# Kernel tuning notes

Hardware: AMD Instinct MI355X
Metric: run time of the kernel (lower is better)

## Reference

```python
import jax, jax.numpy as jnp
import numpy as np

D_MODEL = 1024
N_LAYERS = 2
D_INNER = 2048   # expand_factor * d_model
D_STATE = 16
DT_RANK = 64     # ceil(d_model/16)
D_CONV = 4
BATCH = 2
SEQ = 1024
EPS = 1e-5


def setup_inputs() -> dict:
    key = jax.random.key(0)
    ks = jax.random.split(key, 8)
    s = 0.02
    x = jax.random.normal(ks[0], (BATCH, SEQ, D_MODEL), jnp.float32)
    norm_w = jnp.ones((N_LAYERS, D_MODEL), jnp.float32)
    in_proj_w = jax.random.normal(ks[1], (N_LAYERS, 2 * D_INNER, D_MODEL), jnp.float32) * s
    conv_w = jax.random.normal(ks[2], (N_LAYERS, D_INNER, D_CONV), jnp.float32) * s  # depthwise kernel
    conv_b = jnp.zeros((N_LAYERS, D_INNER), jnp.float32)
    x_proj_w = jax.random.normal(ks[3], (N_LAYERS, DT_RANK + 2 * D_STATE, D_INNER), jnp.float32) * s
    dt_std = DT_RANK ** -0.5
    dt_proj_w = jax.random.uniform(ks[4], (N_LAYERS, D_INNER, DT_RANK), jnp.float32, -dt_std, dt_std)
    dt = jnp.exp(jax.random.uniform(ks[5], (N_LAYERS, D_INNER), jnp.float32)
                 * (np.log(0.1) - np.log(0.001)) + np.log(0.001))
    dt = jnp.clip(dt, 1e-4)
    dt_proj_b = dt + jnp.log(-jnp.expm1(-dt))  # inverse softplus init
    A_log = jnp.broadcast_to(jnp.log(jnp.arange(1, D_STATE + 1, dtype=jnp.float32)),
                             (N_LAYERS, D_INNER, D_STATE)).copy()
    D_param = jnp.ones((N_LAYERS, D_INNER), jnp.float32)
    out_proj_w = jax.random.normal(ks[6], (N_LAYERS, D_MODEL, D_INNER), jnp.float32) * s
    return dict(x=x, norm_w=norm_w, in_proj_w=in_proj_w, conv_w=conv_w, conv_b=conv_b,
                x_proj_w=x_proj_w, dt_proj_w=dt_proj_w, dt_proj_b=dt_proj_b,
                A_log=A_log, D_param=D_param, out_proj_w=out_proj_w)


def _rms_norm(x, w):
    return x * jax.lax.rsqrt(jnp.mean(x * x, axis=-1, keepdims=True) + EPS) * w


def _silu(x):
    return x * jax.nn.sigmoid(x)


def _mamba_block(x, in_w, cw, cb, xp_w, dt_w, dt_b, A_log, Dp, out_w):
    # x: (B, L, D)
    xz = x @ in_w.T                      # (B, L, 2*ED)
    xc, z = jnp.split(xz, 2, axis=-1)    # each (B, L, ED)
    # causal depthwise conv1d (torch pads d_conv-1 both sides then slices [:L])
    xpad = jnp.pad(xc, ((0, 0), (D_CONV - 1, 0), (0, 0)))
    L = xc.shape[1]
    xc = sum(xpad[:, k:k + L, :] * cw[:, k] for k in range(D_CONV)) + cb
    xc = _silu(xc)
    # projections for delta, B, C
    dbc = xc @ xp_w.T                    # (B, L, dt_rank + 2N)
    delta = dbc[..., :DT_RANK]
    Bm = dbc[..., DT_RANK:DT_RANK + D_STATE]
    Cm = dbc[..., DT_RANK + D_STATE:]
    delta = jax.nn.softplus(delta @ dt_w.T + dt_b)      # (B, L, ED)
    A = -jnp.exp(A_log)                                 # (ED, N)
    dA = jnp.exp(delta[..., None] * A)                  # (B, L, ED, N)
    bx = (delta * xc)[..., None] * Bm[:, :, None, :]    # (B, L, ED, N)

    def combine(e1, e2):
        a1, b1 = e1
        a2, b2 = e2
        return a2 * a1, a2 * b1 + b2

    _, hs = jax.lax.associative_scan(combine, (dA, bx), axis=1)  # h_t = dA_t*h_{t-1} + bx_t
    y = jnp.einsum('blen,bln->ble', hs, Cm) + Dp * xc
    return (y * _silu(z)) @ out_w.T


def reference(x, norm_w, in_proj_w, conv_w, conv_b, x_proj_w, dt_proj_w, dt_proj_b,
              A_log, D_param, out_proj_w):
    for i in range(N_LAYERS):
        h = _rms_norm(x, norm_w[i])
        x = x + _mamba_block(h, in_proj_w[i], conv_w[i], conv_b[i], x_proj_w[i],
                             dt_proj_w[i], dt_proj_b[i], A_log[i], D_param[i], out_proj_w[i])
    return x
```

## Files before the change

kernel.cpp:

```cpp
#include <hip/hip_runtime.h>
#include <hip/hip_bf16.h>

#define BATCH   2
#define SEQ     1024
#define DMODEL  1024
#define DINNER  2048
#define DSTATE  16
#define DTRANK  64
#define DCONV   4
#define NLAYERS 2
#define ROWS    (BATCH*SEQ)
#define NCHUNK  32
#define CHUNK   32
#define KSPLIT  8
#define KSLICE  (DINNER / KSPLIT)
#define KSO     4
#define KSLICE_O (DINNER / KSO)

typedef unsigned short ushort_t;
typedef __attribute__((ext_vector_type(8))) short short8;
typedef __attribute__((ext_vector_type(4))) float f32x4;

__device__ __forceinline__ ushort_t f2bf(float f) {
  union { float f; unsigned u; } v; v.f = f;
  unsigned r = v.u + 0x7fffu + ((v.u >> 16) & 1u);
  return (ushort_t)(r >> 16);
}
__device__ __forceinline__ float bf2f(ushort_t h) {
  union { unsigned u; float f; } v; v.u = ((unsigned)h) << 16;
  return v.f;
}

__device__ __forceinline__ void g2lds16(const ushort_t* g, ushort_t* l) {
  __builtin_amdgcn_global_load_lds(
      (const __attribute__((address_space(1))) void*)g,
      (__attribute__((address_space(3))) void*)l, 16, 0, 0);
}

__device__ __forceinline__ void xcd_swz(int& bx, int& by) {
  const int nx = gridDim.x, nwg = nx * gridDim.y;
  int id = by * nx + bx;
  const int q = nwg >> 3;
  id = (id & 7) * q + (id >> 3);
  bx = id % nx; by = id / nx;
}

#define STG_Q(tid) (((tid) & 3) ^ (((tid) >> 3) & 3))
#define LDQ(lane)  ((((lane) >> 4) ^ (((lane) >> 1) & 3)) * 8)

__global__ __launch_bounds__(256) void cast_bf16_kernel(
    const float* __restrict__ in, ushort_t* __restrict__ out)
{
  const int i = blockIdx.x * 256 + threadIdx.x;
  const float4 v = reinterpret_cast<const float4*>(in)[i];
  ushort4 o;
  o.x = f2bf(v.x); o.y = f2bf(v.y); o.z = f2bf(v.z); o.w = f2bf(v.w);
  reinterpret_cast<ushort4*>(out)[i] = o;
}

__global__ __launch_bounds__(256) void rmsnorm_kernel(
    const float* __restrict__ x, const float* __restrict__ w,
    ushort_t* __restrict__ out)
{
  const int row = blockIdx.x;
  const float* xr = x + (size_t)row * DMODEL;
  float ss = 0.f;
  #pragma unroll
  for (int i = threadIdx.x; i < DMODEL; i += 256) { float v = xr[i]; ss += v * v; }
  #pragma unroll
  for (int m = 1; m < 64; m <<= 1) ss += __shfl_xor(ss, m);
  __shared__ float red[4];
  if ((threadIdx.x & 63) == 0) red[threadIdx.x >> 6] = ss;
  __syncthreads();
  float tot = red[0] + red[1] + red[2] + red[3];
  float scale = rsqrtf(tot * (1.f / DMODEL) + 1e-5f);
  #pragma unroll
  for (int i = threadIdx.x; i < DMODEL; i += 256)
    out[(size_t)row * DMODEL + i] = f2bf(xr[i] * scale * w[i]);
}

template<int MODE>
__global__ __launch_bounds__(256) void gemm_bf16_kernel(
    const ushort_t* __restrict__ A, const ushort_t* __restrict__ B,
    ushort_t* __restrict__ C2, const float* __restrict__ bias,
    int K, int lda, int ldb, int ldc)
{
  __shared__ __align__(16) ushort_t As[128 * 32];
  __shared__ __align__(16) ushort_t Bs[128 * 32];
  const int tid = threadIdx.x;
  const int lane = tid & 63, wid = tid >> 6;
  const int wr = wid >> 1, wc = wid & 1;
  int bx = blockIdx.x, by = blockIdx.y;
  xcd_swz(bx, by);
  const int row0 = by * 128, col0 = bx * 128;

  const int sq = STG_Q(tid) * 8;
  const ushort_t* ga0 = A + (size_t)(row0 + (tid >> 2)) * lda + sq;
  const ushort_t* ga1 = A + (size_t)(row0 + 64 + (tid >> 2)) * lda + sq;
  const ushort_t* gb0 = B + (size_t)(col0 + (tid >> 2)) * ldb + sq;
  const ushort_t* gb1 = B + (size_t)(col0 + 64 + (tid >> 2)) * ldb + sq;
  ushort_t* la0 = &As[tid * 8];
  ushort_t* la1 = &As[(256 + tid) * 8];
  ushort_t* lb0 = &Bs[tid * 8];
  ushort_t* lb1 = &Bs[(256 + tid) * 8];

  const int lk = LDQ(lane);
  const int lr16 = lane & 15;

  f32x4 acc[4][4] = {};

  for (int kb = 0; kb < K; kb += 32) {
    g2lds16(ga0 + kb, la0);
    g2lds16(ga1 + kb, la1);
    g2lds16(gb0 + kb, lb0);
    g2lds16(gb1 + kb, lb1);
    __syncthreads();

    short8 af[4], bfr[4];
    #pragma unroll
    for (int i = 0; i < 4; ++i)
      af[i] = *reinterpret_cast<const short8*>(
          &As[(wr * 64 + i * 16 + lr16) * 32 + lk]);
    #pragma unroll
    for (int j = 0; j < 4; ++j)
      bfr[j] = *reinterpret_cast<const short8*>(
          &Bs[(wc * 64 + j * 16 + lr16) * 32 + lk]);
    #pragma unroll
    for (int i = 0; i < 4; ++i)
      #pragma unroll
      for (int j = 0; j < 4; ++j)
        acc[i][j] = __builtin_amdgcn_mfma_f32_16x16x32_bf16(
            af[i], bfr[j], acc[i][j], 0, 0, 0);
    __syncthreads();
  }

  const int cr = (lane >> 4) * 4;
  #pragma unroll
  for (int i = 0; i < 4; ++i) {
    #pragma unroll
    for (int j = 0; j < 4; ++j) {
      const int col = col0 + wc * 64 + j * 16 + lr16;
      #pragma unroll
      for (int r = 0; r < 4; ++r) {
        const int row = row0 + wr * 64 + i * 16 + cr + r;
        float v = acc[i][j][r];
        if (MODE == 3) {
          v += bias[col];
          v = (v > 20.f) ? v : log1pf(__expf(v));
        }
        C2[(size_t)row * ldc + col] = f2bf(v);
      }
    }
  }
}

__global__ __launch_bounds__(256) void outproj_splitk_kernel(
    const ushort_t* __restrict__ A,
    const ushort_t* __restrict__ B,
    ushort_t* __restrict__ partial)
{
  __shared__ __align__(16) ushort_t As[128 * 32];
  __shared__ __align__(16) ushort_t Bs[128 * 32];
  const int tid = threadIdx.x;
  const int lane = tid & 63, wid = tid >> 6;
  const int wr = wid >> 1, wc = wid & 1;
  int bx = blockIdx.x, by = blockIdx.y;
  xcd_swz(bx, by);
  const int row0 = by * 128, col0 = bx * 128;
  const int k0 = blockIdx.z * KSLICE_O;

  const int sq = STG_Q(tid) * 8;
  const ushort_t* ga0 = A + (size_t)(row0 + (tid >> 2)) * DINNER + k0 + sq;
  const ushort_t* ga1 = A + (size_t)(row0 + 64 + (tid >> 2)) * DINNER + k0 + sq;
  const ushort_t* gb0 = B + (size_t)(col0 + (tid >> 2)) * DINNER + k0 + sq;
  const ushort_t* gb1 = B + (size_t)(col0 + 64 + (tid >> 2)) * DINNER + k0 + sq;
  ushort_t* la0 = &As[tid * 8];
  ushort_t* la1 = &As[(256 + tid) * 8];
  ushort_t* lb0 = &Bs[tid * 8];
  ushort_t* lb1 = &Bs[(256 + tid) * 8];

  const int lk = LDQ(lane);
  const int lr16 = lane & 15;

  f32x4 acc[4][4] = {};

  for (int kb = 0; kb < KSLICE_O; kb += 32) {
    g2lds16(ga0 + kb, la0);
    g2lds16(ga1 + kb, la1);
    g2lds16(gb0 + kb, lb0);
    g2lds16(gb1 + kb, lb1);
    __syncthreads();

    short8 af[4], bfr[4];
    #pragma unroll
    for (int i = 0; i < 4; ++i)
      af[i] = *reinterpret_cast<const short8*>(
          &As[(wr * 64 + i * 16 + lr16) * 32 + lk]);
    #pragma unroll
    for (int j = 0; j < 4; ++j)
      bfr[j] = *reinterpret_cast<const short8*>(
          &Bs[(wc * 64 + j * 16 + lr16) * 32 + lk]);
    #pragma unroll
    for (int i = 0; i < 4; ++i)
      #pragma unroll
      for (int j = 0; j < 4; ++j)
        acc[i][j] = __builtin_amdgcn_mfma_f32_16x16x32_bf16(
            af[i], bfr[j], acc[i][j], 0, 0, 0);
    __syncthreads();
  }

  ushort_t* Cz = partial + (size_t)blockIdx.z * ROWS * DMODEL;
  const int cr = (lane >> 4) * 4;
  #pragma unroll
  for (int i = 0; i < 4; ++i) {
    #pragma unroll
    for (int j = 0; j < 4; ++j) {
      const int col = col0 + wc * 64 + j * 16 + lr16;
      #pragma unroll
      for (int r = 0; r < 4; ++r) {
        const int row = row0 + wr * 64 + i * 16 + cr + r;
        Cz[(size_t)row * DMODEL + col] = f2bf(acc[i][j][r]);
      }
    }
  }
}

__global__ __launch_bounds__(256) void outproj_reduce_kernel(
    const ushort_t* __restrict__ partial, float* __restrict__ out)
{
  const int i = blockIdx.x * 256 + threadIdx.x;
  float4 s = reinterpret_cast<float4*>(out)[i];
  #pragma unroll
  for (int z = 0; z < KSO; ++z) {
    const ushort4 p = reinterpret_cast<const ushort4*>(
        partial + (size_t)z * ROWS * DMODEL)[i];
    s.x += bf2f(p.x); s.y += bf2f(p.y); s.z += bf2f(p.z); s.w += bf2f(p.w);
  }
  reinterpret_cast<float4*>(out)[i] = s;
}

__global__ __launch_bounds__(256) void xproj_mfma_kernel(
    const ushort_t* __restrict__ A,
    const ushort_t* __restrict__ B,
    ushort_t* __restrict__ partial)
{
  __shared__ __align__(16) ushort_t As[128 * 32];
  __shared__ __align__(16) ushort_t Bs[96 * 32];
  const int tid = threadIdx.x;
  const int lane = tid & 63, wid = tid >> 6;
  int bx = blockIdx.x, by = blockIdx.y;
  xcd_swz(bx, by);
  const int kz = bx, row0 = by * 128;
  const int k0 = kz * KSLICE;

  const int sq = STG_Q(tid) * 8;
  const ushort_t* ga0 = A + (size_t)(row0 + (tid >> 2)) * DINNER + k0 + sq;
  const ushort_t* ga1 = A + (size_t)(row0 + 64 + (tid >> 2)) * DINNER + k0 + sq;
  const ushort_t* gb0 = B + (size_t)(tid >> 2) * DINNER + k0 + sq;
  const ushort_t* gb1 = B + (size_t)(64 + (tid >> 2)) * DINNER + k0 + sq;
  ushort_t* la0 = &As[tid * 8];
  ushort_t* la1 = &As[(256 + tid) * 8];
  ushort_t* lb0 = &Bs[tid * 8];
  ushort_t* lb1 = &Bs[(256 + tid) * 8];

  const int lk = LDQ(lane);
  const int lr16 = lane & 15;

  f32x4 acc[2][6] = {};

  for (int kb = 0; kb < KSLICE; kb += 32) {
    g2lds16(ga0 + kb, la0);
    g2lds16(ga1 + kb, la1);
    g2lds16(gb0 + kb, lb0);
    if (tid < 128) g2lds16(gb1 + kb, lb1);
    __syncthreads();

    short8 af[2], bfr[6];
    #pragma unroll
    for (int i = 0; i < 2; ++i)
      af[i] = *reinterpret_cast<const short8*>(
          &As[(wid * 32 + i * 16 + lr16) * 32 + lk]);
    #pragma unroll
    for (int j = 0; j < 6; ++j)
      bfr[j] = *reinterpret_cast<const short8*>(
          &Bs[(j * 16 + lr16) * 32 + lk]);
    #pragma unroll
    for (int i = 0; i < 2; ++i)
      #pragma unroll
      for (int j = 0; j < 6; ++j)
        acc[i][j] = __builtin_amdgcn_mfma_f32_16x16x32_bf16(
            af[i], bfr[j], acc[i][j], 0, 0, 0);
    __syncthreads();
  }

  const int cr = (lane >> 4) * 4;
  #pragma unroll
  for (int i = 0; i < 2; ++i) {
    #pragma unroll
    for (int j = 0; j < 6; ++j) {
      const int col = j * 16 + lr16;
      #pragma unroll
      for (int r = 0; r < 4; ++r) {
        const int row = row0 + wid * 32 + i * 16 + cr + r;
        partial[((size_t)kz * ROWS + row) * 96 + col] = f2bf(acc[i][j][r]);
      }
    }
  }
}

__global__ __launch_bounds__(256) void xproj_reduce_kernel(
    const ushort_t* __restrict__ partial, float* __restrict__ dbcBC,
    ushort_t* __restrict__ dl16)
{
  const int idx = blockIdx.x * 256 + threadIdx.x;
  const int row = idx / 96, j = idx % 96;
  float s = 0.f;
  #pragma unroll
  for (int z = 0; z < KSPLIT; ++z)
    s += bf2f(partial[(size_t)z * ROWS * 96 + idx]);
  if (j < DTRANK) dl16[row * DTRANK + j] = f2bf(s);
  else            dbcBC[row * 32 + (j - DTRANK)] = s;
}

__global__ __launch_bounds__(256) void conv_silu_kernel(
    const ushort_t* __restrict__ xz16,
    const float* __restrict__ cw, const float* __restrict__ cb,
    ushort_t* __restrict__ xc16)
{
  const int idx = blockIdx.x * 256 + threadIdx.x;
  const int e0 = (idx * 8) % DINNER;
  const int bl = (idx * 8) / DINNER;
  const int l  = bl % SEQ;
  float acc[8];
  #pragma unroll
  for (int j = 0; j < 8; ++j) acc[j] = cb[e0 + j];
  float4 w4[8];
  #pragma unroll
  for (int j = 0; j < 8; ++j)
    w4[j] = *reinterpret_cast<const float4*>(&cw[(e0 + j) * DCONV]);
  #pragma unroll
  for (int k = 0; k < DCONV; ++k) {
    const int lk = l + k - (DCONV - 1);
    if (lk >= 0) {
      const short8 v = *reinterpret_cast<const short8*>(
          &xz16[(size_t)(bl + k - (DCONV - 1)) * (2 * DINNER) + e0]);
      #pragma unroll
      for (int j = 0; j < 8; ++j) {
        const float wv = (k == 0) ? w4[j].x : (k == 1) ? w4[j].y
                        : (k == 2) ? w4[j].z : w4[j].w;
        acc[j] += bf2f((ushort_t)v[j]) * wv;
      }
    }
  }
  short8 o;
  #pragma unroll
  for (int j = 0; j < 8; ++j) {
    const float v = acc[j] / (1.f + __expf(-acc[j]));
    o[j] = (short)f2bf(v);
  }
  *reinterpret_cast<short8*>(&xc16[(size_t)bl * DINNER + e0]) = o;
}

__global__ __launch_bounds__(256) void scan_chunk_kernel(
    const ushort_t* __restrict__ d16,
    const ushort_t* __restrict__ xc16,
    const float* __restrict__ dbcBC,
    const float* __restrict__ A_log,
    float* __restrict__ Pbuf,
    float* __restrict__ Hbuf)
{
  __shared__ float sB[CHUNK][16];
  const int bc = blockIdx.y;
  const int b = bc / NCHUNK, c = bc % NCHUNK;
  const int e = blockIdx.x * 256 + threadIdx.x;
  const size_t row32 = ((size_t)b * SEQ + c * CHUNK) * 32;
  #pragma unroll
  for (int p = 0; p < (CHUNK * 16) / 256; ++p) {
    const int idx = threadIdx.x + p * 256;
    sB[idx >> 4][idx & 15] = dbcBC[row32 + (idx >> 4) * 32 + (idx & 15)];
  }
  float Aen[16];
  #pragma unroll
  for (int q = 0; q < 4; ++q) {
    const float4 a4 = *reinterpret_cast<const float4*>(&A_log[(size_t)e * 16 + q * 4]);
    Aen[q * 4 + 0] = -__expf(a4.x);
    Aen[q * 4 + 1] = -__expf(a4.y);
    Aen[q * 4 + 2] = -__expf(a4.z);
    Aen[q * 4 + 3] = -__expf(a4.w);
  }
  __syncthreads();

  float h[16];
  #pragma unroll
  for (int n = 0; n < 16; ++n) h[n] = 0.f;
  float sd = 0.f;
  const size_t rowE = ((size_t)b * SEQ + c * CHUNK) * DINNER + e;
  float dv = bf2f(d16[rowE]), xv = bf2f(xc16[rowE]);
  for (int t = 0; t < CHUNK; ++t) {
    float dvn = 0.f, xvn = 0.f;
    if (t + 1 < CHUNK) {
      dvn = bf2f(d16[rowE + (size_t)(t + 1) * DINNER]);
      xvn = bf2f(xc16[rowE + (size_t)(t + 1) * DINNER]);
    }
    const float dxv = dv * xv;
    sd += dv;
    #pragma unroll
    for (int n = 0; n < 16; ++n) {
      const float dA = __expf(dv * Aen[n]);
      h[n] = dA * h[n] + dxv * sB[t][n];
    }
    dv = dvn; xv = xvn;
  }
  const size_t o = ((size_t)bc * DINNER + e) * 16;
  #pragma unroll
  for (int q = 0; q < 4; ++q) {
    float4 pv, hv;
    pv.x = __expf(Aen[q * 4 + 0] * sd);
    pv.y = __expf(Aen[q * 4 + 1] * sd);
    pv.z = __expf(Aen[q * 4 + 2] * sd);
    pv.w = __expf(Aen[q * 4 + 3] * sd);
    hv.x = h[q * 4 + 0]; hv.y = h[q * 4 + 1];
    hv.z = h[q * 4 + 2]; hv.w = h[q * 4 + 3];
    *reinterpret_cast<float4*>(&Pbuf[o + q * 4]) = pv;
    *reinterpret_cast<float4*>(&Hbuf[o + q * 4]) = hv;
  }
}

__global__ __launch_bounds__(256) void scan_combine_kernel(
    const float* __restrict__ Pbuf, float* __restrict__ Hbuf)
{
  const int idx = blockIdx.x * 256 + threadIdx.x;
  const int b = idx >> 15;
  const int en = idx & (DINNER * 16 - 1);
  const size_t base = (size_t)b * NCHUNK * DINNER * 16 + en;
  float H = 0.f;
  float P = Pbuf[base], hf = Hbuf[base];
  for (int c = 0; c < NCHUNK; ++c) {
    const size_t o = base + (size_t)c * DINNER * 16;
    float Pn = 0.f, hfn = 0.f;
    if (c + 1 < NCHUNK) {
      const size_t on = o + (size_t)DINNER * 16;
      Pn = Pbuf[on]; hfn = Hbuf[on];
    }
    Hbuf[o] = H;
    H = P * H + hf;
    P = Pn; hf = hfn;
  }
}

__global__ __launch_bounds__(256) void scan_out_kernel(
    const ushort_t* __restrict__ d16,
    const ushort_t* __restrict__ xc16,
    const float* __restrict__ dbcBC,
    const ushort_t* __restrict__ xz16,
    const float* __restrict__ A_log,
    const float* __restrict__ Dp,
    const float* __restrict__ Hbuf,
    ushort_t* __restrict__ yz16)
{
  __shared__ float sB[CHUNK][16];
  __shared__ float sC[CHUNK][16];
  const int bc = blockIdx.y;
  const int b = bc / NCHUNK, c = bc % NCHUNK;
  const int e = blockIdx.x * 256 + threadIdx.x;
  const size_t row32 = ((size_t)b * SEQ + c * CHUNK) * 32;
  #pragma unroll
  for (int p = 0; p < (CHUNK * 32) / 256; ++p) {
    const int idx = threadIdx.x + p * 256;
    const int t = idx >> 5, j = idx & 31;
    const float v = dbcBC[row32 + t * 32 + j];
    if (j < 16) sB[t][j] = v; else sC[t][j - 16] = v;
  }
  float Aen[16];
  #pragma unroll
  for (int q = 0; q < 4; ++q) {
    const float4 a4 = *reinterpret_cast<const float4*>(&A_log[(size_t)e * 16 + q * 4]);
    Aen[q * 4 + 0] = -__expf(a4.x);
    Aen[q * 4 + 1] = -__expf(a4.y);
    Aen[q * 4 + 2] = -__expf(a4.z);
    Aen[q * 4 + 3] = -__expf(a4.w);
  }
  float h[16];
  const size_t oh = ((size_t)bc * DINNER + e) * 16;
  #pragma unroll
  for (int q = 0; q < 4; ++q) {
    const float4 hv = *reinterpret_cast<const float4*>(&Hbuf[oh + q * 4]);
    h[q * 4 + 0] = hv.x; h[q * 4 + 1] = hv.y;
    h[q * 4 + 2] = hv.z; h[q * 4 + 3] = hv.w;
  }
  const float dpe = Dp[e];
  __syncthreads();

  const size_t rowE = ((size_t)b * SEQ + c * CHUNK) * DINNER + e;
  const size_t rowZ = ((size_t)b * SEQ + c * CHUNK) * (2 * DINNER) + DINNER + e;
  float dv = bf2f(d16[rowE]), xv = bf2f(xc16[rowE]);
  float zv = bf2f(xz16[rowZ]);
  for (int t = 0; t < CHUNK; ++t) {
    float dvn = 0.f, xvn = 0.f, zvn = 0.f;
    if (t + 1 < CHUNK) {
      dvn = bf2f(d16[rowE + (size_t)(t + 1) * DINNER]);
      xvn = bf2f(xc16[rowE + (size_t)(t + 1) * DINNER]);
      zvn = bf2f(xz16[rowZ + (size_t)(t + 1) * (2 * DINNER)]);
    }
    const float dxv = dv * xv;
    float y = dpe * xv;
    #pragma unroll
    for (int n = 0; n < 16; ++n) {
      const float dA = __expf(dv * Aen[n]);
      h[n] = dA * h[n] + dxv * sB[t][n];
      y += h[n] * sC[t][n];
    }
    const float sz = zv / (1.f + __expf(-zv));
    yz16[rowE + (size_t)t * DINNER] = f2bf(y * sz);
    dv = dvn; xv = xvn; zv = zvn;
  }
}

extern "C" void kernel_launch(void* const* d_in, const int* in_sizes, int n_in,
                              void* d_out, int out_size, void* d_ws, size_t ws_size,
                              hipStream_t stream)
{
  const float* x         = (const float*)d_in[0];
  const float* norm_w    = (const float*)d_in[1];
  const float* in_proj_w = (const float*)d_in[2];
  const float* conv_w    = (const float*)d_in[3];
  const float* conv_b    = (const float*)d_in[4];
  const float* x_proj_w  = (const float*)d_in[5];
  const float* dt_proj_w = (const float*)d_in[6];
  const float* dt_proj_b = (const float*)d_in[7];
  const float* A_log     = (const float*)d_in[8];
  const float* D_param   = (const float*)d_in[9];
  const float* out_proj_w= (const float*)d_in[10];
  float* out = (float*)d_out;

  const size_t M = 1024 * 1024;
  float* ws = (float*)d_ws;
  ushort_t* h16   = (ushort_t*)ws;
  ushort_t* w16i  = (ushort_t*)(ws + 1 * M);
  ushort_t* partO = (ushort_t*)ws;
  ushort_t* w16o  = (ushort_t*)(ws + 4 * M);
  ushort_t* xz16  = (ushort_t*)(ws + 5 * M);
  ushort_t* xc16  = (ushort_t*)(ws + 9 * M);
  ushort_t* d16   = (ushort_t*)(ws + 11 * M);
  float* P_buf    = ws + 13 * M;
  ushort_t* yz16  = (ushort_t*)P_buf;
  float* H_buf    = ws + 15 * M;
  ushort_t* partX = (ushort_t*)(ws + 17 * M);
  ushort_t* xpw16 = (ushort_t*)(ws + 17 * M + 786432);
  ushort_t* dtw16 = (ushort_t*)(ws + 17 * M + 786432 + 98304);
  float* dbcBC    = ws + 17 * M + 786432 + 98304 + 65536;
  ushort_t* dl16  = (ushort_t*)(dbcBC + 65536);

  hipMemcpyAsync(out, x, (size_t)ROWS * DMODEL * sizeof(float),
                 hipMemcpyDeviceToDevice, stream);

  for (int layer = 0; layer < NLAYERS; ++layer) {
    const float* nw  = norm_w     + (size_t)layer * DMODEL;
    const float* iw  = in_proj_w  + (size_t)layer * 2 * DINNER * DMODEL;
    const float* cw  = conv_w     + (size_t)layer * DINNER * DCONV;
    const float* cb  = conv_b     + (size_t)layer * DINNER;
    const float* xpw = x_proj_w   + (size_t)layer * 96 * DINNER;
    const float* dtw = dt_proj_w  + (size_t)layer * DINNER * DTRANK;
    const float* dtb = dt_proj_b  + (size_t)layer * DINNER;
    const float* Al  = A_log      + (size_t)layer * DINNER * DSTATE;
    const float* Dpp = D_param    + (size_t)layer * DINNER;
    const float* ow  = out_proj_w + (size_t)layer * DMODEL * DINNER;

    rmsnorm_kernel<<<ROWS, 256, 0, stream>>>(out, nw, h16);

    cast_bf16_kernel<<<(2 * DINNER * DMODEL) / 1024, 256, 0, stream>>>(iw, w16i);

    gemm_bf16_kernel<2>
        <<<dim3(2 * DINNER / 128, ROWS / 128), 256, 0, stream>>>(
            h16, w16i, xz16, nullptr, DMODEL, DMODEL, DMODEL, 2 * DINNER);

    conv_silu_kernel<<<(size_t)ROWS * DINNER / 8 / 256, 256, 0, stream>>>(
        xz16, cw, cb, xc16);

    cast_bf16_kernel<<<(96 * DINNER) / 1024, 256, 0, stream>>>(xpw, xpw16);
    cast_bf16_kernel<<<(DINNER * DTRANK) / 1024, 256, 0, stream>>>(dtw, dtw16);

    xproj_mfma_kernel<<<dim3(KSPLIT, ROWS / 128), 256, 0, stream>>>(
        xc16, xpw16, partX);
    xproj_reduce_kernel<<<ROWS * 96 / 256, 256, 0, stream>>>(
        partX, dbcBC, dl16);

    gemm_bf16_kernel<3>
        <<<dim3(DINNER / 128, ROWS / 128), 256, 0, stream>>>(
            dl16, dtw16, d16, dtb, DTRANK, DTRANK, DTRANK, DINNER);

    scan_chunk_kernel<<<dim3(DINNER / 256, BATCH * NCHUNK), 256, 0, stream>>>(
        d16, xc16, dbcBC, Al, P_buf, H_buf);
    scan_combine_kernel<<<BATCH * DINNER * 16 / 256, 256, 0, stream>>>(
        P_buf, H_buf);
    scan_out_kernel<<<dim3(DINNER / 256, BATCH * NCHUNK), 256, 0, stream>>>(
        d16, xc16, dbcBC, xz16, Al, Dpp, H_buf, yz16);

    cast_bf16_kernel<<<(DMODEL * DINNER) / 1024, 256, 0, stream>>>(ow, w16o);

    outproj_splitk_kernel
        <<<dim3(DMODEL / 128, ROWS / 128, KSO), 256, 0, stream>>>(
            yz16, w16o, partO);
    outproj_reduce_kernel<<<ROWS * DMODEL / 1024, 256, 0, stream>>>(
        partO, out);
  }
}
```

Measured before the change: 344.5 us.

## Fuse RMSNorm into residual reduce, batch weight casts, store scan carries in bf16

Merges the initial copy with the first RMSNorm, and folds each later RMSNorm into the out-projection split-K reduce kernel, so the residual is not read again per layer. All weight casts for both layers are issued up front in four launches instead of per-layer casts. The scan chunk prefix products and carry states are stored as bf16 instead of fp32, halving that scratch traffic at some cost in accuracy of the cross-chunk recurrence. The workspace layout is rearranged to fit the new buffers.

```diff
diff --git a/kernel.cpp b/kernel.cpp
--- a/kernel.cpp
+++ b/kernel.cpp
@@ -58,25 +58,27 @@
   reinterpret_cast<ushort4*>(out)[i] = o;
 }
 
-__global__ __launch_bounds__(256) void rmsnorm_kernel(
+__global__ __launch_bounds__(256) void init_rms_kernel(
     const float* __restrict__ x, const float* __restrict__ w,
-    ushort_t* __restrict__ out)
-{
-  const int row = blockIdx.x;
-  const float* xr = x + (size_t)row * DMODEL;
-  float ss = 0.f;
-  #pragma unroll
-  for (int i = threadIdx.x; i < DMODEL; i += 256) { float v = xr[i]; ss += v * v; }
+    float* __restrict__ out, ushort_t* __restrict__ h16)
+{
+  const int row = blockIdx.x, t = threadIdx.x;
+  const size_t base = (size_t)row * DMODEL + 4 * t;
+  const float4 s = *reinterpret_cast<const float4*>(&x[base]);
+  *reinterpret_cast<float4*>(&out[base]) = s;
+  float ss = s.x * s.x + s.y * s.y + s.z * s.z + s.w * s.w;
   #pragma unroll
   for (int m = 1; m < 64; m <<= 1) ss += __shfl_xor(ss, m);
   __shared__ float red[4];
-  if ((threadIdx.x & 63) == 0) red[threadIdx.x >> 6] = ss;
+  if ((t & 63) == 0) red[t >> 6] = ss;
   __syncthreads();
-  float tot = red[0] + red[1] + red[2] + red[3];
-  float scale = rsqrtf(tot * (1.f / DMODEL) + 1e-5f);
-  #pragma unroll
-  for (int i = threadIdx.x; i < DMODEL; i += 256)
-    out[(size_t)row * DMODEL + i] = f2bf(xr[i] * scale * w[i]);
+  const float tot = red[0] + red[1] + red[2] + red[3];
+  const float scale = rsqrtf(tot * (1.f / DMODEL) + 1e-5f);
+  const float4 w4 = *reinterpret_cast<const float4*>(&w[4 * t]);
+  ushort4 o;
+  o.x = f2bf(s.x * scale * w4.x); o.y = f2bf(s.y * scale * w4.y);
+  o.z = f2bf(s.z * scale * w4.z); o.w = f2bf(s.w * scale * w4.w);
+  *reinterpret_cast<ushort4*>(&h16[base]) = o;
 }
 
 template<int MODE>
@@ -225,18 +227,36 @@
   }
 }
 
-__global__ __launch_bounds__(256) void outproj_reduce_kernel(
-    const ushort_t* __restrict__ partial, float* __restrict__ out)
-{
-  const int i = blockIdx.x * 256 + threadIdx.x;
-  float4 s = reinterpret_cast<float4*>(out)[i];
+template<bool RMS>
+__global__ __launch_bounds__(256) void outproj_reduce_rms_kernel(
+    const ushort_t* __restrict__ partial, const float* __restrict__ nw,
+    float* __restrict__ out, ushort_t* __restrict__ h16)
+{
+  const int row = blockIdx.x, t = threadIdx.x;
+  const size_t base = (size_t)row * DMODEL + 4 * t;
+  float4 s = *reinterpret_cast<float4*>(&out[base]);
   #pragma unroll
   for (int z = 0; z < KSO; ++z) {
-    const ushort4 p = reinterpret_cast<const ushort4*>(
-        partial + (size_t)z * ROWS * DMODEL)[i];
+    const ushort4 p = *reinterpret_cast<const ushort4*>(
+        &partial[(size_t)z * ROWS * DMODEL + base]);
     s.x += bf2f(p.x); s.y += bf2f(p.y); s.z += bf2f(p.z); s.w += bf2f(p.w);
   }
-  reinterpret_cast<float4*>(out)[i] = s;
+  *reinterpret_cast<float4*>(&out[base]) = s;
+  if (RMS) {
+    float ss = s.x * s.x + s.y * s.y + s.z * s.z + s.w * s.w;
+    #pragma unroll
+    for (int m = 1; m < 64; m <<= 1) ss += __shfl_xor(ss, m);
+    __shared__ float red[4];
+    if ((t & 63) == 0) red[t >> 6] = ss;
+    __syncthreads();
+    const float tot = red[0] + red[1] + red[2] + red[3];
+    const float scale = rsqrtf(tot * (1.f / DMODEL) + 1e-5f);
+    const float4 w4 = *reinterpret_cast<const float4*>(&nw[4 * t]);
+    ushort4 o;
+    o.x = f2bf(s.x * scale * w4.x); o.y = f2bf(s.y * scale * w4.y);
+    o.z = f2bf(s.z * scale * w4.z); o.w = f2bf(s.w * scale * w4.w);
+    *reinterpret_cast<ushort4*>(&h16[base]) = o;
+  }
 }
 
 __global__ __launch_bounds__(256) void xproj_mfma_kernel(
@@ -366,8 +386,8 @@
     const ushort_t* __restrict__ xc16,
     const float* __restrict__ dbcBC,
     const float* __restrict__ A_log,
-    float* __restrict__ Pbuf,
-    float* __restrict__ Hbuf)
+    ushort_t* __restrict__ P16,
+    ushort_t* __restrict__ H16)
 {
   __shared__ float sB[CHUNK][16];
   const int bc = blockIdx.y;
@@ -414,35 +434,35 @@
   const size_t o = ((size_t)bc * DINNER + e) * 16;
   #pragma unroll
   for (int q = 0; q < 4; ++q) {
-    float4 pv, hv;
-    pv.x = __expf(Aen[q * 4 + 0] * sd);
-    pv.y = __expf(Aen[q * 4 + 1] * sd);
-    pv.z = __expf(Aen[q * 4 + 2] * sd);
-    pv.w = __expf(Aen[q * 4 + 3] * sd);
-    hv.x = h[q * 4 + 0]; hv.y = h[q * 4 + 1];
-    hv.z = h[q * 4 + 2]; hv.w = h[q * 4 + 3];
-    *reinterpret_cast<float4*>(&Pbuf[o + q * 4]) = pv;
-    *reinterpret_cast<float4*>(&Hbuf[o + q * 4]) = hv;
+    ushort4 pv, hv;
+    pv.x = f2bf(__expf(Aen[q * 4 + 0] * sd));
+    pv.y = f2bf(__expf(Aen[q * 4 + 1] * sd));
+    pv.z = f2bf(__expf(Aen[q * 4 + 2] * sd));
+    pv.w = f2bf(__expf(Aen[q * 4 + 3] * sd));
+    hv.x = f2bf(h[q * 4 + 0]); hv.y = f2bf(h[q * 4 + 1]);
+    hv.z = f2bf(h[q * 4 + 2]); hv.w = f2bf(h[q * 4 + 3]);
+    *reinterpret_cast<ushort4*>(&P16[o + q * 4]) = pv;
+    *reinterpret_cast<ushort4*>(&H16[o + q * 4]) = hv;
   }
 }
 
 __global__ __launch_bounds__(256) void scan_combine_kernel(
-    const float* __restrict__ Pbuf, float* __restrict__ Hbuf)
+    const ushort_t* __restrict__ P16, ushort_t* __restrict__ H16)
 {
   const int idx = blockIdx.x * 256 + threadIdx.x;
   const int b = idx >> 15;
   const int en = idx & (DINNER * 16 - 1);
   const size_t base = (size_t)b * NCHUNK * DINNER * 16 + en;
   float H = 0.f;
-  float P = Pbuf[base], hf = Hbuf[base];
+  float P = bf2f(P16[base]), hf = bf2f(H16[base]);
   for (int c = 0; c < NCHUNK; ++c) {
     const size_t o = base + (size_t)c * DINNER * 16;
     float Pn = 0.f, hfn = 0.f;
     if (c + 1 < NCHUNK) {
       const size_t on = o + (size_t)DINNER * 16;
-      Pn = Pbuf[on]; hfn = Hbuf[on];
-    }
-    Hbuf[o] = H;
+      Pn = bf2f(P16[on]); hfn = bf2f(H16[on]);
+    }
+    H16[o] = f2bf(H);
     H = P * H + hf;
     P = Pn; hf = hfn;
   }
@@ -455,7 +475,7 @@
     const ushort_t* __restrict__ xz16,
     const float* __restrict__ A_log,
     const float* __restrict__ Dp,
-    const float* __restrict__ Hbuf,
+    const ushort_t* __restrict__ H16,
     ushort_t* __restrict__ yz16)
 {
   __shared__ float sB[CHUNK][16];
@@ -484,9 +504,9 @@
   const size_t oh = ((size_t)bc * DINNER + e) * 16;
   #pragma unroll
   for (int q = 0; q < 4; ++q) {
-    const float4 hv = *reinterpret_cast<const float4*>(&Hbuf[oh + q * 4]);
-    h[q * 4 + 0] = hv.x; h[q * 4 + 1] = hv.y;
-    h[q * 4 + 2] = hv.z; h[q * 4 + 3] = hv.w;
+    const ushort4 hv = *reinterpret_cast<const ushort4*>(&H16[oh + q * 4]);
+    h[q * 4 + 0] = bf2f(hv.x); h[q * 4 + 1] = bf2f(hv.y);
+    h[q * 4 + 2] = bf2f(hv.z); h[q * 4 + 3] = bf2f(hv.w);
   }
   const float dpe = Dp[e];
   __syncthreads();
@@ -535,40 +555,43 @@
 
   const size_t M = 1024 * 1024;
   float* ws = (float*)d_ws;
-  ushort_t* h16   = (ushort_t*)ws;
-  ushort_t* w16i  = (ushort_t*)(ws + 1 * M);
-  ushort_t* partO = (ushort_t*)ws;
-  ushort_t* w16o  = (ushort_t*)(ws + 4 * M);
-  ushort_t* xz16  = (ushort_t*)(ws + 5 * M);
-  ushort_t* xc16  = (ushort_t*)(ws + 9 * M);
-  ushort_t* d16   = (ushort_t*)(ws + 11 * M);
-  float* P_buf    = ws + 13 * M;
-  ushort_t* yz16  = (ushort_t*)P_buf;
-  float* H_buf    = ws + 15 * M;
-  ushort_t* partX = (ushort_t*)(ws + 17 * M);
-  ushort_t* xpw16 = (ushort_t*)(ws + 17 * M + 786432);
-  ushort_t* dtw16 = (ushort_t*)(ws + 17 * M + 786432 + 98304);
-  float* dbcBC    = ws + 17 * M + 786432 + 98304 + 65536;
-  ushort_t* dl16  = (ushort_t*)(dbcBC + 65536);
-
-  hipMemcpyAsync(out, x, (size_t)ROWS * DMODEL * sizeof(float),
-                 hipMemcpyDeviceToDevice, stream);
+  ushort_t* w16i_all = (ushort_t*)ws;
+  ushort_t* w16o_all = (ushort_t*)(ws + 4 * M);
+  ushort_t* xpw16_all= (ushort_t*)(ws + 6 * M);
+  ushort_t* dtw16_all= (ushort_t*)(ws + 6 * M + 196608);
+  float* dbcBC    = ws + 6 * M + 327680;
+  ushort_t* dl16  = (ushort_t*)(ws + 6 * M + 393216);
+  ushort_t* xz16  = (ushort_t*)(ws + 6 * M + 524288);
+  ushort_t* partO = xz16;
+  ushort_t* xc16  = (ushort_t*)(ws + 10 * M + 524288);
+  ushort_t* d16   = (ushort_t*)(ws + 12 * M + 524288);
+  ushort_t* P16   = (ushort_t*)(ws + 14 * M + 524288);
+  ushort_t* H16   = (ushort_t*)(ws + 15 * M + 524288);
+  ushort_t* yz16  = (ushort_t*)(ws + 16 * M + 524288);
+  ushort_t* h16   = (ushort_t*)(ws + 18 * M + 524288);
+  ushort_t* partX = (ushort_t*)(ws + 19 * M + 524288);
+
+  cast_bf16_kernel<<<NLAYERS * 2 * DINNER * DMODEL / 1024, 256, 0, stream>>>(
+      in_proj_w, w16i_all);
+  cast_bf16_kernel<<<NLAYERS * DMODEL * DINNER / 1024, 256, 0, stream>>>(
+      out_proj_w, w16o_all);
+  cast_bf16_kernel<<<NLAYERS * 96 * DINNER / 1024, 256, 0, stream>>>(
+      x_proj_w, xpw16_all);
+  cast_bf16_kernel<<<NLAYERS * DINNER * DTRANK / 1024, 256, 0, stream>>>(
+      dt_proj_w, dtw16_all);
+
+  init_rms_kernel<<<ROWS, 256, 0, stream>>>(x, norm_w, out, h16);
 
   for (int layer = 0; layer < NLAYERS; ++layer) {
-    const float* nw  = norm_w     + (size_t)layer * DMODEL;
-    const float* iw  = in_proj_w  + (size_t)layer * 2 * DINNER * DMODEL;
     const float* cw  = conv_w     + (size_t)layer * DINNER * DCONV;
     const float* cb  = conv_b     + (size_t)layer * DINNER;
-    const float* xpw = x_proj_w   + (size_t)layer * 96 * DINNER;
-    const float* dtw = dt_proj_w  + (size_t)layer * DINNER * DTRANK;
     const float* dtb = dt_proj_b  + (size_t)layer * DINNER;
     const float* Al  = A_log      + (size_t)layer * DINNER * DSTATE;
     const float* Dpp = D_param    + (size_t)layer * DINNER;
-    const float* ow  = out_proj_w + (size_t)layer * DMODEL * DINNER;
-
-    rmsnorm_kernel<<<ROWS, 256, 0, stream>>>(out, nw, h16);
-
-    cast_bf16_kernel<<<(2 * DINNER * DMODEL) / 1024, 256, 0, stream>>>(iw, w16i);
+    const ushort_t* w16i  = w16i_all  + (size_t)layer * 2 * DINNER * DMODEL;
+    const ushort_t* w16o  = w16o_all  + (size_t)layer * DMODEL * DINNER;
+    const ushort_t* xpw16 = xpw16_all + (size_t)layer * 96 * DINNER;
+    const ushort_t* dtw16 = dtw16_all + (size_t)layer * DINNER * DTRANK;
 
     gemm_bf16_kernel<2>
         <<<dim3(2 * DINNER / 128, ROWS / 128), 256, 0, stream>>>(
@@ -576,9 +599,6 @@
 
     conv_silu_kernel<<<(size_t)ROWS * DINNER / 8 / 256, 256, 0, stream>>>(
         xz16, cw, cb, xc16);
-
-    cast_bf16_kernel<<<(96 * DINNER) / 1024, 256, 0, stream>>>(xpw, xpw16);
-    cast_bf16_kernel<<<(DINNER * DTRANK) / 1024, 256, 0, stream>>>(dtw, dtw16);
 
     xproj_mfma_kernel<<<dim3(KSPLIT, ROWS / 128), 256, 0, stream>>>(
         xc16, xpw16, partX);
@@ -590,18 +610,22 @@
             dl16, dtw16, d16, dtb, DTRANK, DTRANK, DTRANK, DINNER);
 
     scan_chunk_kernel<<<dim3(DINNER / 256, BATCH * NCHUNK), 256, 0, stream>>>(
-        d16, xc16, dbcBC, Al, P_buf, H_buf);
+        d16, xc16, dbcBC, Al, P16, H16);
     scan_combine_kernel<<<BATCH * DINNER * 16 / 256, 256, 0, stream>>>(
-        P_buf, H_buf);
+        P16, H16);
     scan_out_kernel<<<dim3(DINNER / 256, BATCH * NCHUNK), 256, 0, stream>>>(
-        d16, xc16, dbcBC, xz16, Al, Dpp, H_buf, yz16);
-
-    cast_bf16_kernel<<<(DMODEL * DINNER) / 1024, 256, 0, stream>>>(ow, w16o);
+        d16, xc16, dbcBC, xz16, Al, Dpp, H16, yz16);
 
     outproj_splitk_kernel
         <<<dim3(DMODEL / 128, ROWS / 128, KSO), 256, 0, stream>>>(
             yz16, w16o, partO);
-    outproj_reduce_kernel<<<ROWS * DMODEL / 1024, 256, 0, stream>>>(
-        partO, out);
-  }
-}
+
+    if (layer + 1 < NLAYERS) {
+      outproj_reduce_rms_kernel<true><<<ROWS, 256, 0, stream>>>(
+          partO, norm_w + (size_t)(layer + 1) * DMODEL, out, h16);
+    } else {
+      outproj_reduce_rms_kernel<false><<<ROWS, 256, 0, stream>>>(
+          partO, nullptr, out, nullptr);
+    }
+  }
+}
```

New measurement: 315.2 us. 8.5% less time.
